# Optimization experiments

Measured on AMD Instinct MI355X. Metric: run time of the kernel, lower is better.

The kernel has to match this reference:

```python
import math
import jax, jax.numpy as jnp
import numpy as np

B, S, H = 2, 2048, 2048
N_HEADS, N_KV_HEADS = 16, 4
HEAD_DIM = H // N_HEADS  # 128
ROPE_BASE = 10000.0


def setup_inputs() -> dict:
    key = jax.random.key(0)
    ks = jax.random.split(key, 8)
    hidden_states = jax.random.normal(ks[0], (B, S, H), dtype=jnp.float32)
    # continuous, increasing timestamps in [0, S)
    time_values = jnp.sort(jax.random.uniform(ks[1], (B, S), dtype=jnp.float32) * S, axis=-1)
    sc = 1.0 / math.sqrt(H)
    wq = jax.random.normal(ks[2], (H, N_HEADS * HEAD_DIM), dtype=jnp.float32) * sc
    bq = jnp.zeros((N_HEADS * HEAD_DIM,), dtype=jnp.float32)
    wk = jax.random.normal(ks[3], (H, N_KV_HEADS * HEAD_DIM), dtype=jnp.float32) * sc
    bk = jnp.zeros((N_KV_HEADS * HEAD_DIM,), dtype=jnp.float32)
    wv = jax.random.normal(ks[4], (H, N_KV_HEADS * HEAD_DIM), dtype=jnp.float32) * sc
    bv = jnp.zeros((N_KV_HEADS * HEAD_DIM,), dtype=jnp.float32)
    wo = jax.random.normal(ks[5], (N_HEADS * HEAD_DIM, H), dtype=jnp.float32) * sc
    # learnable per-dimension frequency modulation (init ones, as in module)
    rope_w = jnp.ones((HEAD_DIM // 2,), dtype=jnp.float32)
    return {"hidden_states": hidden_states, "time_values": time_values,
            "wq": wq, "bq": bq, "wk": wk, "bk": bk, "wv": wv, "bv": bv,
            "wo": wo, "rope_w": rope_w}


def _rotate_half(x):
    x1, x2 = jnp.split(x, 2, axis=-1)
    return jnp.concatenate((-x2, x1), axis=-1)


def reference(hidden_states, time_values, wq, bq, wk, bk, wv, bv, wo, rope_w):
    b, s, h = hidden_states.shape
    # QKV projections -> [b, heads, s, head_dim]
    q = (hidden_states @ wq + bq).reshape(b, s, N_HEADS, HEAD_DIM).transpose(0, 2, 1, 3)
    k = (hidden_states @ wk + bk).reshape(b, s, N_KV_HEADS, HEAD_DIM).transpose(0, 2, 1, 3)
    v = (hidden_states @ wv + bv).reshape(b, s, N_KV_HEADS, HEAD_DIM).transpose(0, 2, 1, 3)
    # Continuous-time RoPE: freqs = t * inv_freq * w  -> [b, s, hd/2]
    inv_freq = 1.0 / (ROPE_BASE ** (jnp.arange(0, HEAD_DIM, 2, dtype=jnp.float32) / HEAD_DIM))
    freqs = time_values[:, :, None] * inv_freq * rope_w
    emb = jnp.concatenate((freqs, freqs), axis=-1)[:, None]  # [b, 1, s, hd]
    cos = jnp.cos(emb).astype(q.dtype)
    sin = jnp.sin(emb).astype(q.dtype)
    q = q * cos + _rotate_half(q) * sin
    k = k * cos + _rotate_half(k) * sin
    # GQA: repeat_kv
    n_rep = N_HEADS // N_KV_HEADS
    k = jnp.repeat(k, n_rep, axis=1)
    v = jnp.repeat(v, n_rep, axis=1)
    # scaled dot-product attention, causal
    scale = 1.0 / math.sqrt(HEAD_DIM)
    scores = jnp.einsum('bhqd,bhkd->bhqk', q, k) * scale
    causal = jnp.tril(jnp.ones((s, s), dtype=bool))
    scores = jnp.where(causal, scores, jnp.finfo(scores.dtype).min)
    attn = jax.nn.softmax(scores, axis=-1)
    out = jnp.einsum('bhqk,bhkd->bhqd', attn, v)  # [b, nh, s, hd]
    out = out.transpose(0, 2, 1, 3).reshape(b, s, N_HEADS * HEAD_DIM)
    return out @ wo
```

## Files before the change

### kernel.cpp

```cpp
#include <hip/hip_runtime.h>


#define S_LEN 2048
#define BATCH 2
#define NH    16
#define NKV   4
#define HD    128

typedef float  f32x4  __attribute__((ext_vector_type(4)));
typedef __bf16 bf16x8 __attribute__((ext_vector_type(8)));
typedef __bf16 bf16x4 __attribute__((ext_vector_type(4)));
typedef unsigned int u32x4 __attribute__((ext_vector_type(4)));
typedef unsigned int u32x2 __attribute__((ext_vector_type(2)));

__device__ inline unsigned short f2bf(float f) {
    unsigned u = __builtin_bit_cast(unsigned, f);
    unsigned r = (u + 0x7fffu + ((u >> 16) & 1u)) >> 16;
    return (unsigned short)r;
}

__device__ inline void gload_lds16(const void* g, void* l) {
    __builtin_amdgcn_global_load_lds(
        (const __attribute__((address_space(1))) unsigned int*)g,
        (__attribute__((address_space(3))) unsigned int*)l, 16, 0, 0);
}

__global__ void transpose_qkv(const float* __restrict__ wq,
                              const float* __restrict__ wk,
                              const float* __restrict__ wv,
                              unsigned short* __restrict__ Wt) {
    int z = blockIdx.z;
    const float* src = (z == 0) ? wq : ((z == 1) ? wk : wv);
    int C = (z == 0) ? 2048 : 512;
    long doff = (z == 0) ? 0L : ((z == 1) ? 2048L * 2048 : 2560L * 2048);
    int bx = blockIdx.x * 32, by = blockIdx.y * 32;
    if (bx >= C) return;
    __shared__ unsigned short t[32][33];
    int x = threadIdx.x, y0 = threadIdx.y;
    #pragma unroll
    for (int i = 0; i < 4; i++) {
        int y = y0 + i * 8;
        t[y][x] = f2bf(src[(long)(by + y) * C + bx + x]);
    }
    __syncthreads();
    #pragma unroll
    for (int i = 0; i < 4; i++) {
        int y = y0 + i * 8;
        Wt[doff + (long)(bx + y) * 2048 + by + x] = t[x][y];
    }
}

__global__ void transpose_to_bf16(const float* __restrict__ src,
                                  unsigned short* __restrict__ dst,
                                  int R, int C, long dst_off, int ldd) {
    __shared__ unsigned short t[32][33];
    int bx = blockIdx.x * 32, by = blockIdx.y * 32;
    int x = threadIdx.x, y0 = threadIdx.y;
    #pragma unroll
    for (int i = 0; i < 4; i++) {
        int y = y0 + i * 8;
        t[y][x] = f2bf(src[(long)(by + y) * C + bx + x]);
    }
    __syncthreads();
    #pragma unroll
    for (int i = 0; i < 4; i++) {
        int y = y0 + i * 8;
        dst[dst_off + (long)(bx + y) * ldd + by + x] = t[x][y];
    }
}

__global__ __launch_bounds__(256) void prep_kernel(
        const float* __restrict__ X, unsigned short* __restrict__ Xb,
        const float* __restrict__ bq, const float* __restrict__ bk,
        const float* __restrict__ bv, float* __restrict__ bsf,
        const float* __restrict__ tv, const float* __restrict__ rw,
        unsigned int* __restrict__ Tab) {
    int bi = blockIdx.x, tid = threadIdx.x;
    long i = ((long)bi * 256 + tid) * 8;
    {
        f32x4 a = *(const f32x4*)&X[i];
        f32x4 b = *(const f32x4*)&X[i + 4];
        u32x4 r;
        r.x = (unsigned)f2bf(a[0]) | ((unsigned)f2bf(a[1]) << 16);
        r.y = (unsigned)f2bf(a[2]) | ((unsigned)f2bf(a[3]) << 16);
        r.z = (unsigned)f2bf(b[0]) | ((unsigned)f2bf(b[1]) << 16);
        r.w = (unsigned)f2bf(b[2]) | ((unsigned)f2bf(b[3]) << 16);
        *(u32x4*)&Xb[i] = r;
    }
    if (bi < 12) {
        int ib = bi * 256 + tid;
        bsf[ib] = (ib < 2048) ? bq[ib] : ((ib < 2560) ? bk[ib - 2048] : bv[ib - 2560]);
    }
    if (bi < 1024) {
        int m = bi * 4 + (tid >> 6);
        int fi = tid & 63;
        float t = tv[m];
        float f = t * powf(10000.f, -(float)fi / 64.f) * rw[fi];
        Tab[m * 64 + fi] = (unsigned)f2bf(cosf(f)) | ((unsigned)f2bf(sinf(f)) << 16);
    }
}

__global__ __launch_bounds__(256) void gemm_qkv_rope(
        const unsigned short* __restrict__ A,
        const unsigned short* __restrict__ Bt,
        const float* __restrict__ bsf,
        const unsigned int* __restrict__ Tab,
        unsigned short* __restrict__ Qr,
        unsigned short* __restrict__ Kr,
        unsigned short* __restrict__ Vt) {
    __shared__ __align__(16) char smem[32768];
    unsigned short* As = (unsigned short*)smem;
    unsigned short* Bs = (unsigned short*)(smem + 16384);
    float* Ep = (float*)smem;

    const int tid = threadIdx.x;
    const int wid = tid >> 6, lane = tid & 63, quad = lane >> 4, l16 = lane & 15;
    const int wr = wid >> 1, wc = wid & 1;
    const int m0 = blockIdx.y * 128, n0 = blockIdx.x * 128;
    const int bx = blockIdx.x;
    const int l7 = l16 & 7;

    f32x4 acc[4][4];
    #pragma unroll
    for (int i = 0; i < 4; i++)
        #pragma unroll
        for (int j = 0; j < 4; j++)
            #pragma unroll
            for (int c = 0; c < 4; c++) acc[i][j][c] = 0.f;

    for (int k0 = 0; k0 < 2048; k0 += 64) {
        #pragma unroll
        for (int i = 0; i < 4; i++) {
            int c = tid + 256 * i;
            int row = c >> 3, loct = ((c & 7) ^ (row & 7)) * 8;
            gload_lds16(&A[(long)(m0 + row) * 2048 + k0 + loct], &As[c * 8]);
        }
        #pragma unroll
        for (int i = 0; i < 4; i++) {
            int c = tid + 256 * i;
            int row = c >> 3, loct = ((c & 7) ^ (row & 7)) * 8;
            gload_lds16(&Bt[(long)(n0 + row) * 2048 + k0 + loct], &Bs[c * 8]);
        }
        __syncthreads();
        #pragma unroll
        for (int s = 0; s < 2; s++) {
            bf16x8 af[4], bfr[4];
            #pragma unroll
            for (int mi = 0; mi < 4; mi++)
                af[mi] = *(const bf16x8*)
                    &As[(wr * 64 + mi * 16 + l16) * 64 + (((s * 4 + quad) ^ l7)) * 8];
            #pragma unroll
            for (int ni = 0; ni < 4; ni++)
                bfr[ni] = *(const bf16x8*)
                    &Bs[(wc * 64 + ni * 16 + l16) * 64 + (((s * 4 + quad) ^ l7)) * 8];
            #pragma unroll
            for (int mi = 0; mi < 4; mi++)
                #pragma unroll
                for (int ni = 0; ni < 4; ni++)
                    acc[mi][ni] = __builtin_amdgcn_mfma_f32_16x16x32_bf16(
                        af[mi], bfr[ni], acc[mi][ni], 0, 0, 0);
        }
        __syncthreads();
    }

    float bv4[4];
    #pragma unroll
    for (int ni = 0; ni < 4; ni++) bv4[ni] = bsf[n0 + wc * 64 + ni * 16 + l16];
    const bool isV = (bx >= 20);
    const float qs = (bx < 16) ? (0.08838834764831845f * 1.4426950408889634f) : 1.0f;

    const int lr = tid >> 3, jj = tid & 7, j0 = jj * 8;

    u32x4 tq[4][2];
    if (!isV) {
        #pragma unroll
        for (int mi = 0; mi < 4; mi++) {
            int gm = m0 + ((lr >> 4) << 6) + mi * 16 + (lr & 15);
            tq[mi][0] = *(const u32x4*)&Tab[(long)gm * 64 + j0];
            tq[mi][1] = *(const u32x4*)&Tab[(long)gm * 64 + j0 + 4];
        }
    }

    #pragma unroll
    for (int mi = 0; mi < 4; mi++) {
        #pragma unroll
        for (int ni = 0; ni < 4; ni++)
            #pragma unroll
            for (int r = 0; r < 4; r++)
                Ep[(wr * 16 + quad * 4 + r) * 132 + wc * 64 + ni * 16 + l16] =
                    acc[mi][ni][r] + bv4[ni];
        __syncthreads();
        if (!isV) {
            const int gm = m0 + ((lr >> 4) << 6) + mi * 16 + (lr & 15);
            const int bb = gm >> 11, s = gm & 2047;
            unsigned short* dst = (bx < 16)
                ? Qr + ((long)(bb * NH + bx) * S_LEN + s) * HD
                : Kr + ((long)(bb * NKV + (bx - 16)) * S_LEN + s) * HD;
            f32x4 x1a = *(f32x4*)&Ep[lr * 132 + j0];
            f32x4 x1b = *(f32x4*)&Ep[lr * 132 + j0 + 4];
            f32x4 x2a = *(f32x4*)&Ep[lr * 132 + 64 + j0];
            f32x4 x2b = *(f32x4*)&Ep[lr * 132 + 64 + j0 + 4];
            f32x4 la, lb, ha, hb;
            #pragma unroll
            for (int e = 0; e < 4; e++) {
                float ca = __builtin_bit_cast(float, tq[mi][0][e] << 16);
                float sa = __builtin_bit_cast(float, tq[mi][0][e] & 0xffff0000u);
                float cb = __builtin_bit_cast(float, tq[mi][1][e] << 16);
                float sb = __builtin_bit_cast(float, tq[mi][1][e] & 0xffff0000u);
                la[e] = (x1a[e] * ca - x2a[e] * sa) * qs;
                ha[e] = (x2a[e] * ca + x1a[e] * sa) * qs;
                lb[e] = (x1b[e] * cb - x2b[e] * sb) * qs;
                hb[e] = (x2b[e] * cb + x1b[e] * sb) * qs;
            }
            u32x4 lo, hi;
            lo.x = (unsigned)f2bf(la[0]) | ((unsigned)f2bf(la[1]) << 16);
            lo.y = (unsigned)f2bf(la[2]) | ((unsigned)f2bf(la[3]) << 16);
            lo.z = (unsigned)f2bf(lb[0]) | ((unsigned)f2bf(lb[1]) << 16);
            lo.w = (unsigned)f2bf(lb[2]) | ((unsigned)f2bf(lb[3]) << 16);
            hi.x = (unsigned)f2bf(ha[0]) | ((unsigned)f2bf(ha[1]) << 16);
            hi.y = (unsigned)f2bf(ha[2]) | ((unsigned)f2bf(ha[3]) << 16);
            hi.z = (unsigned)f2bf(hb[0]) | ((unsigned)f2bf(hb[1]) << 16);
            hi.w = (unsigned)f2bf(hb[2]) | ((unsigned)f2bf(hb[3]) << 16);
            *(u32x4*)&dst[j0] = lo;
            *(u32x4*)&dst[64 + j0] = hi;
        } else {
            const int d = tid >> 1, sh = tid & 1;
            const int gmb = m0 + sh * 64 + mi * 16;
            const int bb = gmb >> 11, s0 = gmb & 2047;
            unsigned short* dst =
                Vt + ((long)(bb * NKV + (bx - 20)) * HD + d) * S_LEN + s0;
            unsigned short pv[16];
            #pragma unroll
            for (int t = 0; t < 16; t++)
                pv[t] = f2bf(Ep[(sh * 16 + t) * 132 + d]);
            u32x4 v0, v1;
            v0.x = (unsigned)pv[0]  | ((unsigned)pv[1]  << 16);
            v0.y = (unsigned)pv[2]  | ((unsigned)pv[3]  << 16);
            v0.z = (unsigned)pv[4]  | ((unsigned)pv[5]  << 16);
            v0.w = (unsigned)pv[6]  | ((unsigned)pv[7]  << 16);
            v1.x = (unsigned)pv[8]  | ((unsigned)pv[9]  << 16);
            v1.y = (unsigned)pv[10] | ((unsigned)pv[11] << 16);
            v1.z = (unsigned)pv[12] | ((unsigned)pv[13] << 16);
            v1.w = (unsigned)pv[14] | ((unsigned)pv[15] << 16);
            *(u32x4*)&dst[0] = v0;
            *(u32x4*)&dst[8] = v1;
        }
        __syncthreads();
    }
}

template <typename CT>
__global__ __launch_bounds__(256) void gemm_bt_async(
        const unsigned short* __restrict__ A,
        const unsigned short* __restrict__ Bt,
        CT* __restrict__ C,
        const float* __restrict__ bias,
        int K, int lda, int ldb, int ldc) {
    __shared__ __align__(16) unsigned short As[128 * 64];
    __shared__ __align__(16) unsigned short Bs[128 * 64];
    const int tid = threadIdx.x;
    const int wid = tid >> 6, lane = tid & 63, quad = lane >> 4, l16 = lane & 15;
    const int wr = wid >> 1, wc = wid & 1;
    const int m0 = blockIdx.y * 128, n0 = blockIdx.x * 128;
    const int l7 = l16 & 7;

    f32x4 acc[4][4];
    #pragma unroll
    for (int i = 0; i < 4; i++)
        #pragma unroll
        for (int j = 0; j < 4; j++)
            #pragma unroll
            for (int c = 0; c < 4; c++) acc[i][j][c] = 0.f;

    for (int k0 = 0; k0 < K; k0 += 64) {
        #pragma unroll
        for (int i = 0; i < 4; i++) {
            int c = tid + 256 * i;
            int row = c >> 3, loct = ((c & 7) ^ (row & 7)) * 8;
            gload_lds16(&A[(long)(m0 + row) * lda + k0 + loct], &As[c * 8]);
        }
        #pragma unroll
        for (int i = 0; i < 4; i++) {
            int c = tid + 256 * i;
            int row = c >> 3, loct = ((c & 7) ^ (row & 7)) * 8;
            gload_lds16(&Bt[(long)(n0 + row) * ldb + k0 + loct], &Bs[c * 8]);
        }
        __syncthreads();
        #pragma unroll
        for (int s = 0; s < 2; s++) {
            bf16x8 af[4], bfr[4];
            #pragma unroll
            for (int mi = 0; mi < 4; mi++)
                af[mi] = *(const bf16x8*)
                    &As[(wr * 64 + mi * 16 + l16) * 64 + (((s * 4 + quad) ^ l7)) * 8];
            #pragma unroll
            for (int ni = 0; ni < 4; ni++)
                bfr[ni] = *(const bf16x8*)
                    &Bs[(wc * 64 + ni * 16 + l16) * 64 + (((s * 4 + quad) ^ l7)) * 8];
            #pragma unroll
            for (int mi = 0; mi < 4; mi++)
                #pragma unroll
                for (int ni = 0; ni < 4; ni++)
                    acc[mi][ni] = __builtin_amdgcn_mfma_f32_16x16x32_bf16(
                        af[mi], bfr[ni], acc[mi][ni], 0, 0, 0);
        }
        __syncthreads();
    }

    #pragma unroll
    for (int mi = 0; mi < 4; mi++) {
        #pragma unroll
        for (int ni = 0; ni < 4; ni++) {
            int gn = n0 + wc * 64 + ni * 16 + l16;
            float bv_ = bias ? bias[gn] : 0.f;
            #pragma unroll
            for (int r = 0; r < 4; r++) {
                int gm = m0 + wr * 64 + mi * 16 + quad * 4 + r;
                float v = acc[mi][ni][r] + bv_;
                if constexpr (sizeof(CT) == 4) C[(long)gm * ldc + gn] = v;
                else                           C[(long)gm * ldc + gn] = f2bf(v);
            }
        }
    }
}

__global__ __launch_bounds__(512, 4) void attn_kernel(
        const unsigned short* __restrict__ Qr,
        const unsigned short* __restrict__ Kr,
        const unsigned short* __restrict__ Vt,
        unsigned short* __restrict__ Out) {
    __shared__ __align__(16) unsigned short Ks[64 * 128];
    __shared__ __align__(16) unsigned short Vs[128 * 64];
    __shared__ __align__(16) unsigned short Ps[8][16 * 68];

    const int h = blockIdx.x, b = blockIdx.z;
    const int qt = b ? blockIdx.y : (int)(gridDim.y - 1 - blockIdx.y);
    const int tid = threadIdx.x, w = tid >> 6, lane = tid & 63;
    const int quad = lane >> 4, l16 = lane & 15;
    const int hk = h >> 2;
    const unsigned short* Qb = Qr + (long)((b * NH + h) * S_LEN) * HD;
    const unsigned short* Kb = Kr + (long)((b * NKV + hk) * S_LEN) * HD;
    const unsigned short* Vb = Vt + (long)((b * NKV + hk) * HD) * S_LEN;
    const int qw = qt * 128 + w * 16;
    const int q  = qw + l16;
    const float MASK_MIN = -3.0e38f;

    bf16x8 qf[4];
    #pragma unroll
    for (int kc = 0; kc < 4; kc++)
        qf[kc] = *(const bf16x8*)&Qb[(long)q * HD + kc * 32 + quad * 8];

    f32x4 o[8];
    #pragma unroll
    for (int db = 0; db < 8; db++)
        #pragma unroll
        for (int c = 0; c < 4; c++) o[db][c] = 0.f;
    float mr = MASK_MIN, lr = 0.f;

    const int sK0 = tid, sK1 = tid + 512;
    const int kR0 = sK0 >> 4, kC0 = ((sK0 & 15) ^ (kR0 & 15)) * 8;
    const int kR1 = sK1 >> 4, kC1 = ((sK1 & 15) ^ (kR1 & 15)) * 8;
    const int vR0 = sK0 >> 3, vC0 = ((sK0 & 7) ^ (vR0 & 7)) * 8;
    const int vR1 = sK1 >> 3, vC1 = ((sK1 & 7) ^ (vR1 & 7)) * 8;

    const int nkt = 2 * qt + 2;
    for (int kt = 0; kt < nkt; kt++) {
        const int k0 = kt * 64;
        __syncthreads();
        gload_lds16(&Kb[(long)(k0 + kR0) * HD + kC0], &Ks[sK0 * 8]);
        gload_lds16(&Kb[(long)(k0 + kR1) * HD + kC1], &Ks[sK1 * 8]);
        gload_lds16(&Vb[(long)vR0 * S_LEN + k0 + vC0], &Vs[sK0 * 8]);
        gload_lds16(&Vb[(long)vR1 * S_LEN + k0 + vC1], &Vs[sK1 * 8]);
        __syncthreads();

        if (k0 > qw + 15) continue;

        f32x4 sc[4];
        #pragma unroll
        for (int nb = 0; nb < 4; nb++) {
            #pragma unroll
            for (int c = 0; c < 4; c++) sc[nb][c] = 0.f;
            #pragma unroll
            for (int kc = 0; kc < 4; kc++) {
                bf16x8 kf = *(const bf16x8*)
                    &Ks[(nb * 16 + l16) * 128 + (((kc * 4 + quad) ^ l16) * 8)];
                sc[nb] = __builtin_amdgcn_mfma_f32_16x16x32_bf16(kf, qf[kc], sc[nb], 0, 0, 0);
            }
        }
        if (k0 + 63 > qw) {
            #pragma unroll
            for (int nb = 0; nb < 4; nb++) {
                int kvb = k0 + nb * 16 + quad * 4;
                #pragma unroll
                for (int r = 0; r < 4; r++)
                    sc[nb][r] = (kvb + r > q) ? MASK_MIN : sc[nb][r];
            }
        }
        float tm = MASK_MIN;
        #pragma unroll
        for (int nb = 0; nb < 4; nb++)
            #pragma unroll
            for (int r = 0; r < 4; r++) tm = fmaxf(tm, sc[nb][r]);
        tm = fmaxf(tm, __shfl_xor(tm, 16));
        tm = fmaxf(tm, __shfl_xor(tm, 32));

        float mn = mr;
        if (__any(tm > mr)) {
            mn = fmaxf(mr, tm);
            float alpha = exp2f(mr - mn);
            mr = mn;
            lr *= alpha;
            #pragma unroll
            for (int db = 0; db < 8; db++)
                #pragma unroll
                for (int c = 0; c < 4; c++) o[db][c] *= alpha;
        }
        float rs = 0.f;
        #pragma unroll
        for (int nb = 0; nb < 4; nb++) {
            float pv0 = exp2f(sc[nb][0] - mn), pv1 = exp2f(sc[nb][1] - mn);
            float pv2 = exp2f(sc[nb][2] - mn), pv3 = exp2f(sc[nb][3] - mn);
            rs += (pv0 + pv1) + (pv2 + pv3);
            bf16x4 pk4 = { (__bf16)pv0, (__bf16)pv1, (__bf16)pv2, (__bf16)pv3 };
            *(bf16x4*)&Ps[w][l16 * 68 + nb * 16 + quad * 4] = pk4;
        }
        rs += __shfl_xor(rs, 16);
        rs += __shfl_xor(rs, 32);
        lr += rs;

        #pragma unroll
        for (int kk = 0; kk < 2; kk++) {
            bf16x8 pf = *(const bf16x8*)&Ps[w][l16 * 68 + kk * 32 + quad * 8];
            #pragma unroll
            for (int db = 0; db < 8; db++) {
                bf16x8 vf = *(const bf16x8*)
                    &Vs[(db * 16 + l16) * 64 + (((kk * 4 + quad) ^ (l16 & 7)) * 8)];
                o[db] = __builtin_amdgcn_mfma_f32_16x16x32_bf16(vf, pf, o[db], 0, 0, 0);
            }
        }
    }

    float inv_l = 1.0f / lr;
    long obase = (long)(b * S_LEN + q) * 2048 + h * 128 + quad * 4;
    #pragma unroll
    for (int db = 0; db < 8; db++) {
        bf16x4 pk4 = { (__bf16)(o[db][0] * inv_l), (__bf16)(o[db][1] * inv_l),
                       (__bf16)(o[db][2] * inv_l), (__bf16)(o[db][3] * inv_l) };
        *(bf16x4*)&Out[obase + db * 16] = pk4;
    }
}

extern "C" void kernel_launch(void* const* d_in, const int* in_sizes, int n_in,
                              void* d_out, int out_size, void* d_ws, size_t ws_size,
                              hipStream_t stream) {
    const float* X  = (const float*)d_in[0];
    const float* tv = (const float*)d_in[1];
    const float* wq = (const float*)d_in[2];
    const float* bq = (const float*)d_in[3];
    const float* wk = (const float*)d_in[4];
    const float* bk = (const float*)d_in[5];
    const float* wv = (const float*)d_in[6];
    const float* bv = (const float*)d_in[7];
    const float* wo = (const float*)d_in[8];
    const float* rw = (const float*)d_in[9];

    char* ws = (char*)d_ws;
    unsigned short* Wt  = (unsigned short*)ws; ws += 3072L * 2048 * 2;
    float*          bsf = (float*)ws;          ws += 3072L * 4;
    unsigned int*   Tab = (unsigned int*)ws;   ws += 4096L * 64 * 4;
    unsigned short* Qr  = (unsigned short*)ws; ws += (long)BATCH * NH  * S_LEN * HD * 2;
    unsigned short* Kr  = (unsigned short*)ws; ws += (long)BATCH * NKV * S_LEN * HD * 2;
    unsigned short* Vt  = (unsigned short*)ws; ws += (long)BATCH * NKV * HD * S_LEN * 2;
    unsigned short* AO  = (unsigned short*)ws; ws += 4096L * 2048 * 2;
    unsigned short* Xb  = AO;

    transpose_qkv<<<dim3(64, 64, 3), dim3(32, 8), 0, stream>>>(wq, wk, wv, Wt);
    prep_kernel<<<4096, 256, 0, stream>>>(X, Xb, bq, bk, bv, bsf, tv, rw, Tab);
    gemm_qkv_rope<<<dim3(24, 32), 256, 0, stream>>>(Xb, Wt, bsf, Tab, Qr, Kr, Vt);
    transpose_to_bf16<<<dim3(64, 64), dim3(32, 8), 0, stream>>>(wo, Wt, 2048, 2048, 0L, 2048);
    attn_kernel<<<dim3(NH, S_LEN / 128, BATCH), 512, 0, stream>>>(Qr, Kr, Vt, AO);
    gemm_bt_async<float><<<dim3(16, 32), 256, 0, stream>>>(
        AO, Wt, (float*)d_out, nullptr, 2048, 2048, 2048, 2048);
}
```

Before: 326.2 us.

## Restructure QKV GEMM into 256x256 tiles with double-buffered 8-phase pipeline

Rewrites the fused QKV+RoPE GEMM to use 256x256 output tiles with 512 threads and a double-buffered 128KB LDS ring. Global-to-LDS loads are interleaved with MFMA phases using explicit waitcnt, barriers and setprio, and the block index is swizzled for L2 locality. The goal is to hide load latency behind compute and raise arithmetic intensity. The cost is a grid of only 192 blocks, which may underfill the CUs, plus heavier register and LDS use that limits occupancy.

```diff
diff --git a/kernel.cpp b/kernel.cpp
--- a/kernel.cpp
+++ b/kernel.cpp
@@ -100,7 +100,55 @@
     }
 }
 
-__global__ __launch_bounds__(256) void gemm_qkv_rope(
+__device__ __forceinline__ void stage_half(const unsigned short* __restrict__ G,
+        int baseRow, long kc, unsigned short* slot, int r0, int c0, int tid) {
+    gload_lds16(&G[(long)(baseRow + r0) * 2048 + kc + c0], &slot[tid * 8]);
+    gload_lds16(&G[(long)(baseRow + r0 + 128) * 2048 + kc + c0], &slot[4096 + tid * 8]);
+}
+
+#define STG_A(buf, ks, kt) \
+    stage_half(A,  m0, (long)(kt) * 64 + (ks) * 32, &sm[(buf) * 16384 + (ks) * 8192], r0s, c0s, tid)
+#define STG_B(buf, ks, kt) \
+    stage_half(Bt, n0, (long)(kt) * 64 + (ks) * 32, &sm[32768 + (buf) * 16384 + (ks) * 8192], r0s, c0s, tid)
+
+#define NOPV ((void)0)
+#define VM6  asm volatile("s_waitcnt vmcnt(6)" ::: "memory")
+
+#define PH(buf, ks, mh, RDB, STG, VM)                                          \
+    {                                                                          \
+        const int sb_ = (buf) * 16384 + (ks) * 8192;                           \
+        bf16x8 a0 = *(const bf16x8*)&sm[sb_ + abase + (mh) * 2048];            \
+        bf16x8 a1 = *(const bf16x8*)&sm[sb_ + abase + (mh) * 2048 + 512];      \
+        bf16x8 a2 = *(const bf16x8*)&sm[sb_ + abase + (mh) * 2048 + 1024];     \
+        bf16x8 a3 = *(const bf16x8*)&sm[sb_ + abase + (mh) * 2048 + 1536];     \
+        if (RDB) {                                                             \
+            b0 = *(const bf16x8*)&sm[sb_ + bbase];                             \
+            b1 = *(const bf16x8*)&sm[sb_ + bbase + 512];                       \
+            b2 = *(const bf16x8*)&sm[sb_ + bbase + 1024];                      \
+            b3 = *(const bf16x8*)&sm[sb_ + bbase + 1536];                      \
+        }                                                                      \
+        STG;                                                                   \
+        VM;                                                                    \
+        __builtin_amdgcn_s_barrier();                                          \
+        asm volatile("s_waitcnt lgkmcnt(0)" ::: "memory");                     \
+        __builtin_amdgcn_sched_barrier(0);                                     \
+        __builtin_amdgcn_s_setprio(1);                                         \
+        _Pragma("unroll") for (int mi = 0; mi < 4; ++mi) {                     \
+            bf16x8 am = (mi == 0) ? a0 : (mi == 1) ? a1 : (mi == 2) ? a2 : a3; \
+            acc[(mh) * 4 + mi][0] = __builtin_amdgcn_mfma_f32_16x16x32_bf16(   \
+                am, b0, acc[(mh) * 4 + mi][0], 0, 0, 0);                       \
+            acc[(mh) * 4 + mi][1] = __builtin_amdgcn_mfma_f32_16x16x32_bf16(   \
+                am, b1, acc[(mh) * 4 + mi][1], 0, 0, 0);                       \
+            acc[(mh) * 4 + mi][2] = __builtin_amdgcn_mfma_f32_16x16x32_bf16(   \
+                am, b2, acc[(mh) * 4 + mi][2], 0, 0, 0);                       \
+            acc[(mh) * 4 + mi][3] = __builtin_amdgcn_mfma_f32_16x16x32_bf16(   \
+                am, b3, acc[(mh) * 4 + mi][3], 0, 0, 0);                       \
+        }                                                                      \
+        __builtin_amdgcn_s_setprio(0);                                         \
+        __builtin_amdgcn_s_barrier();                                          \
+    }
+
+__global__ __launch_bounds__(512, 2) void gemm_qkv_rope(
         const unsigned short* __restrict__ A,
         const unsigned short* __restrict__ Bt,
         const float* __restrict__ bsf,
@@ -108,109 +156,104 @@
         unsigned short* __restrict__ Qr,
         unsigned short* __restrict__ Kr,
         unsigned short* __restrict__ Vt) {
-    __shared__ __align__(16) char smem[32768];
-    unsigned short* As = (unsigned short*)smem;
-    unsigned short* Bs = (unsigned short*)(smem + 16384);
-    float* Ep = (float*)smem;
+    __shared__ __align__(16) unsigned short sm[65536];
 
     const int tid = threadIdx.x;
     const int wid = tid >> 6, lane = tid & 63, quad = lane >> 4, l16 = lane & 15;
-    const int wr = wid >> 1, wc = wid & 1;
-    const int m0 = blockIdx.y * 128, n0 = blockIdx.x * 128;
-    const int bx = blockIdx.x;
-    const int l7 = l16 & 7;
-
-    f32x4 acc[4][4];
-    #pragma unroll
-    for (int i = 0; i < 4; i++)
+    const int wr = wid >> 2, wc = wid & 3;
+
+    const int u   = blockIdx.y * 12 + blockIdx.x;
+    const int swz = (u & 7) * 24 + (u >> 3);
+    const int bx  = swz % 12;
+    const int m0  = (swz / 12) * 256;
+    const int n0  = bx * 256;
+
+    const int sg    = (quad ^ ((l16 >> 1) & 3)) * 8;
+    const int abase = wr * 4096 + l16 * 32 + sg;
+    const int bbase = 32768 + wc * 2048 + l16 * 32 + sg;
+
+    const int r0s = tid >> 2;
+    const int c0s = ((tid & 3) ^ ((r0s >> 1) & 3)) * 8;
+
+    f32x4 acc[8][4];
+    #pragma unroll
+    for (int i = 0; i < 8; i++)
         #pragma unroll
         for (int j = 0; j < 4; j++)
             #pragma unroll
             for (int c = 0; c < 4; c++) acc[i][j][c] = 0.f;
-
-    for (int k0 = 0; k0 < 2048; k0 += 64) {
-        #pragma unroll
-        for (int i = 0; i < 4; i++) {
-            int c = tid + 256 * i;
-            int row = c >> 3, loct = ((c & 7) ^ (row & 7)) * 8;
-            gload_lds16(&A[(long)(m0 + row) * 2048 + k0 + loct], &As[c * 8]);
-        }
-        #pragma unroll
-        for (int i = 0; i < 4; i++) {
-            int c = tid + 256 * i;
-            int row = c >> 3, loct = ((c & 7) ^ (row & 7)) * 8;
-            gload_lds16(&Bt[(long)(n0 + row) * 2048 + k0 + loct], &Bs[c * 8]);
-        }
-        __syncthreads();
-        #pragma unroll
-        for (int s = 0; s < 2; s++) {
-            bf16x8 af[4], bfr[4];
-            #pragma unroll
-            for (int mi = 0; mi < 4; mi++)
-                af[mi] = *(const bf16x8*)
-                    &As[(wr * 64 + mi * 16 + l16) * 64 + (((s * 4 + quad) ^ l7)) * 8];
-            #pragma unroll
-            for (int ni = 0; ni < 4; ni++)
-                bfr[ni] = *(const bf16x8*)
-                    &Bs[(wc * 64 + ni * 16 + l16) * 64 + (((s * 4 + quad) ^ l7)) * 8];
-            #pragma unroll
-            for (int mi = 0; mi < 4; mi++)
+    bf16x8 b0 = {}, b1 = {}, b2 = {}, b3 = {};
+
+    STG_B(0, 0, 0); STG_A(0, 0, 0); STG_B(0, 1, 0); STG_A(0, 1, 0);
+    STG_B(1, 0, 1); STG_A(1, 0, 1); STG_B(1, 1, 1);
+    asm volatile("s_waitcnt vmcnt(6)" ::: "memory");
+    __builtin_amdgcn_s_barrier();
+
+    for (int it = 0; it < 16; ++it) {
+        const int t1  = 2 * it + 1;
+        const int tn0 = (it < 15) ? 2 * it + 2 : 31;
+        const int tn1 = (it < 15) ? 2 * it + 3 : 31;
+        PH(0, 0, 0, 1, STG_A(1, 1, t1),  NOPV);
+        PH(0, 0, 1, 0, STG_B(0, 0, tn0), NOPV);
+        PH(0, 1, 0, 1, STG_A(0, 0, tn0), NOPV);
+        PH(0, 1, 1, 0, STG_B(0, 1, tn0), VM6);
+        PH(1, 0, 0, 1, STG_A(0, 1, tn0), NOPV);
+        PH(1, 0, 1, 0, STG_B(1, 0, tn1), NOPV);
+        PH(1, 1, 0, 1, STG_A(1, 0, tn1), NOPV);
+        PH(1, 1, 1, 0, STG_B(1, 1, tn1), VM6);
+    }
+
+    asm volatile("s_waitcnt vmcnt(0)" ::: "memory");
+    __syncthreads();
+
+    float* Ep = (float*)sm;
+    const int EPLD = 264;
+    float bv4[4];
+    #pragma unroll
+    for (int ni = 0; ni < 4; ++ni) bv4[ni] = bsf[n0 + wc * 64 + ni * 16 + l16];
+    const bool isV = (bx >= 10);
+    const float qs = (bx < 8) ? (0.08838834764831845f * 1.4426950408889634f) : 1.0f;
+
+    const int lt = tid >> 4, hh = (tid >> 3) & 1, jj = tid & 7, j0 = jj * 8;
+    const int vd = tid >> 1, vsh = tid & 1;
+
+    #pragma unroll
+    for (int p = 0; p < 8; ++p) {
+        if (wr == (p >> 2)) {
+            #pragma unroll
+            for (int f = 0; f < 2; ++f) {
                 #pragma unroll
-                for (int ni = 0; ni < 4; ni++)
-                    acc[mi][ni] = __builtin_amdgcn_mfma_f32_16x16x32_bf16(
-                        af[mi], bfr[ni], acc[mi][ni], 0, 0, 0);
-        }
-        __syncthreads();
-    }
-
-    float bv4[4];
-    #pragma unroll
-    for (int ni = 0; ni < 4; ni++) bv4[ni] = bsf[n0 + wc * 64 + ni * 16 + l16];
-    const bool isV = (bx >= 20);
-    const float qs = (bx < 16) ? (0.08838834764831845f * 1.4426950408889634f) : 1.0f;
-
-    const int lr = tid >> 3, jj = tid & 7, j0 = jj * 8;
-
-    u32x4 tq[4][2];
-    if (!isV) {
-        #pragma unroll
-        for (int mi = 0; mi < 4; mi++) {
-            int gm = m0 + ((lr >> 4) << 6) + mi * 16 + (lr & 15);
-            tq[mi][0] = *(const u32x4*)&Tab[(long)gm * 64 + j0];
-            tq[mi][1] = *(const u32x4*)&Tab[(long)gm * 64 + j0 + 4];
-        }
-    }
-
-    #pragma unroll
-    for (int mi = 0; mi < 4; mi++) {
-        #pragma unroll
-        for (int ni = 0; ni < 4; ni++)
-            #pragma unroll
-            for (int r = 0; r < 4; r++)
-                Ep[(wr * 16 + quad * 4 + r) * 132 + wc * 64 + ni * 16 + l16] =
-                    acc[mi][ni][r] + bv4[ni];
+                for (int ni = 0; ni < 4; ++ni)
+                    #pragma unroll
+                    for (int r = 0; r < 4; ++r)
+                        Ep[(f * 16 + quad * 4 + r) * EPLD + wc * 64 + ni * 16 + l16] =
+                            acc[(p & 3) * 2 + f][ni][r] + bv4[ni];
+            }
+        }
         __syncthreads();
         if (!isV) {
-            const int gm = m0 + ((lr >> 4) << 6) + mi * 16 + (lr & 15);
+            const int gm = m0 + p * 32 + lt;
             const int bb = gm >> 11, s = gm & 2047;
-            unsigned short* dst = (bx < 16)
-                ? Qr + ((long)(bb * NH + bx) * S_LEN + s) * HD
-                : Kr + ((long)(bb * NKV + (bx - 16)) * S_LEN + s) * HD;
-            f32x4 x1a = *(f32x4*)&Ep[lr * 132 + j0];
-            f32x4 x1b = *(f32x4*)&Ep[lr * 132 + j0 + 4];
-            f32x4 x2a = *(f32x4*)&Ep[lr * 132 + 64 + j0];
-            f32x4 x2b = *(f32x4*)&Ep[lr * 132 + 64 + j0 + 4];
+            unsigned short* dst = (bx < 8)
+                ? Qr + ((long)(bb * NH + bx * 2 + hh) * S_LEN + s) * HD
+                : Kr + ((long)(bb * NKV + (bx - 8) * 2 + hh) * S_LEN + s) * HD;
+            u32x4 t0 = *(const u32x4*)&Tab[(long)gm * 64 + j0];
+            u32x4 t1v = *(const u32x4*)&Tab[(long)gm * 64 + j0 + 4];
+            f32x4 x1a = *(f32x4*)&Ep[lt * EPLD + hh * 128 + j0];
+            f32x4 x1b = *(f32x4*)&Ep[lt * EPLD + hh * 128 + j0 + 4];
+            f32x4 x2a = *(f32x4*)&Ep[lt * EPLD + hh * 128 + 64 + j0];
+            f32x4 x2b = *(f32x4*)&Ep[lt * EPLD + hh * 128 + 64 + j0 + 4];
             f32x4 la, lb, ha, hb;
             #pragma unroll
             for (int e = 0; e < 4; e++) {
-                float ca = __builtin_bit_cast(float, tq[mi][0][e] << 16);
-                float sa = __builtin_bit_cast(float, tq[mi][0][e] & 0xffff0000u);
-                float cb = __builtin_bit_cast(float, tq[mi][1][e] << 16);
-                float sb = __builtin_bit_cast(float, tq[mi][1][e] & 0xffff0000u);
+                float ca = __builtin_bit_cast(float, t0[e] << 16);
+                float sa = __builtin_bit_cast(float, t0[e] & 0xffff0000u);
+                float cb = __builtin_bit_cast(float, t1v[e] << 16);
+                float sbv = __builtin_bit_cast(float, t1v[e] & 0xffff0000u);
                 la[e] = (x1a[e] * ca - x2a[e] * sa) * qs;
                 ha[e] = (x2a[e] * ca + x1a[e] * sa) * qs;
-                lb[e] = (x1b[e] * cb - x2b[e] * sb) * qs;
-                hb[e] = (x2b[e] * cb + x1b[e] * sb) * qs;
+                lb[e] = (x1b[e] * cb - x2b[e] * sbv) * qs;
+                hb[e] = (x2b[e] * cb + x1b[e] * sbv) * qs;
             }
             u32x4 lo, hi;
             lo.x = (unsigned)f2bf(la[0]) | ((unsigned)f2bf(la[1]) << 16);
@@ -224,15 +267,14 @@
             *(u32x4*)&dst[j0] = lo;
             *(u32x4*)&dst[64 + j0] = hi;
         } else {
-            const int d = tid >> 1, sh = tid & 1;
-            const int gmb = m0 + sh * 64 + mi * 16;
+            const int gmb = m0 + p * 32 + vsh * 16;
             const int bb = gmb >> 11, s0 = gmb & 2047;
-            unsigned short* dst =
-                Vt + ((long)(bb * NKV + (bx - 20)) * HD + d) * S_LEN + s0;
+            const int vh = (bx - 10) * 2 + (vd >> 7), dl = vd & 127;
+            unsigned short* dst = Vt + ((long)(bb * NKV + vh) * HD + dl) * S_LEN + s0;
             unsigned short pv[16];
             #pragma unroll
-            for (int t = 0; t < 16; t++)
-                pv[t] = f2bf(Ep[(sh * 16 + t) * 132 + d]);
+            for (int t = 0; t < 16; ++t)
+                pv[t] = f2bf(Ep[(vsh * 16 + t) * EPLD + vd]);
             u32x4 v0, v1;
             v0.x = (unsigned)pv[0]  | ((unsigned)pv[1]  << 16);
             v0.y = (unsigned)pv[2]  | ((unsigned)pv[3]  << 16);
@@ -476,7 +518,7 @@
 
     transpose_qkv<<<dim3(64, 64, 3), dim3(32, 8), 0, stream>>>(wq, wk, wv, Wt);
     prep_kernel<<<4096, 256, 0, stream>>>(X, Xb, bq, bk, bv, bsf, tv, rw, Tab);
-    gemm_qkv_rope<<<dim3(24, 32), 256, 0, stream>>>(Xb, Wt, bsf, Tab, Qr, Kr, Vt);
+    gemm_qkv_rope<<<dim3(12, 16), 512, 0, stream>>>(Xb, Wt, bsf, Tab, Qr, Kr, Vt);
     transpose_to_bf16<<<dim3(64, 64), dim3(32, 8), 0, stream>>>(wo, Wt, 2048, 2048, 0L, 2048);
     attn_kernel<<<dim3(NH, S_LEN / 128, BATCH), 512, 0, stream>>>(Qr, Kr, Vt, AO);
     gemm_bt_async<float><<<dim3(16, 32), 256, 0, stream>>>(
```

Result: faster. 303.1 us (-7.1%).
